# Kernel tuning notes

Hardware: AMD Instinct MI355X
Metric: run time of the kernel (lower is better)

Reference implementation:

```python
import jax, jax.numpy as jnp
import numpy as np
import math

NEIGHBOR_RADIUS = 30.0

def _masked_softmax(logits, mask, axis):
    # mask: bool, True = keep; all-masked rows return zeros
    p = jax.nn.softmax(jnp.where(mask, logits, -1e9), axis=axis) * mask.astype(logits.dtype)
    return p / jnp.clip(jnp.sum(p, axis=axis, keepdims=True), 1e-9, None)

def _forward(agents_state, agents_mask, map_polylines, map_poly_mask,
             map_poly_type, map_tl_status, map_on_route,
             pm_w1, pm_b1, pm_w2, pm_b2, type_emb, tl_emb, route_emb,
             mo_w1, mo_b1, mo_w2, mo_b2,
             ae_w1, ae_b1, ae_w2, ae_b2, ae_w3, ae_b3,
             mr_w1, mr_b1, mr_w2, mr_b2,
             nr_w1, nr_b1, nr_w2, nr_b2,
             to_w1, to_b1, to_w2, to_b2):
    relu = jax.nn.relu
    a_mask = (agents_mask > 0.5).astype(agents_state.dtype)   # (B,N,T)
    a_feat = agents_state[..., :5]
    # ---- map polyline node encoder ----
    h = relu(map_polylines @ pm_w1 + pm_b1)                   # (B,M,L,H)
    h = relu(h @ pm_w2 + pm_b2)
    h = h.max(axis=2)                                         # (B,M,H) max-pool over points
    t_idx = jnp.clip(map_poly_type, 0, type_emb.shape[0] - 1)
    s_idx = jnp.clip(map_tl_status, 0, tl_emb.shape[0] - 1)
    r_idx = jnp.clip(map_on_route, 0, route_emb.shape[0] - 1)
    h = h + type_emb[t_idx] + tl_emb[s_idx] + route_emb[r_idx]
    h = relu(h @ mo_w1 + mo_b1) @ mo_w2 + mo_b2
    map_mask = map_poly_mask > 0.5                            # (B,M) bool
    map_node = h * map_mask[..., None].astype(h.dtype)        # (B,M,D)
    map_center = map_polylines.mean(axis=2)                   # (B,M,2)
    # ---- agent state encoder ----
    a = relu(a_feat @ ae_w1 + ae_b1)
    a = relu(a @ ae_w2 + ae_b2)
    a_emb = (a @ ae_w3 + ae_b3) * a_mask[..., None]           # (B,N,T,D)
    D = a_emb.shape[-1]
    # ---- agent -> map attention ----
    agent_pos = a_feat[..., 0:2]
    rel = map_center[:, None, None, :, :] - agent_pos[:, :, :, None, :]  # (B,N,T,M,2)
    dist = jnp.linalg.norm(rel, axis=-1, keepdims=True)
    rel_feat = jnp.concatenate([rel, dist], axis=-1)          # (B,N,T,M,3)
    rel_score = (relu(rel_feat @ mr_w1 + mr_b1) @ mr_w2 + mr_b2)[..., 0]  # (B,N,T,M)
    dot = jnp.einsum('bntd,bmd->bntm', a_emb, map_node) / math.sqrt(D)
    score_mask = jnp.broadcast_to(map_mask[:, None, None, :], dot.shape)
    attn = _masked_softmax(dot + rel_score, score_mask, axis=-1)
    map_ctx = jnp.einsum('bntm,bmd->bntd', attn, map_node)    # (B,N,T,D)
    # ---- neighbor graph attention ----
    pos = a_feat[..., 0:2]
    vel = a_feat[..., 3:5]
    pos_j = jnp.transpose(pos, (0, 2, 1, 3))                  # (B,T,N,2)
    vel_j = jnp.transpose(vel, (0, 2, 1, 3))
    rel_pos = pos_j[:, None, :, :, :] - pos[:, :, :, None, :] # (B,N,T,N,2) = p_j - p_i
    rel_vel = vel_j[:, None, :, :, :] - vel[:, :, :, None, :]
    dist_ij = jnp.linalg.norm(rel_pos, axis=-1, keepdims=True)
    rel_ij = jnp.concatenate([rel_pos, rel_vel, dist_ij], axis=-1)        # (B,N,T,N,5)
    nbr_score = (relu(rel_ij @ nr_w1 + nr_b1) @ nr_w2 + nr_b2)[..., 0]    # (B,N,T,N)
    am_b = agents_mask > 0.5
    valid_i = am_b[..., None]                                 # (B,N,T,1)
    valid_j = jnp.transpose(am_b, (0, 2, 1))[:, None, :, :]   # (B,1,T,N)
    N = pos.shape[1]
    not_self = ~jnp.eye(N, dtype=bool)[None, :, None, :]      # (1,N,1,N)
    nbr_mask = valid_i & valid_j & (dist_ij[..., 0] <= NEIGHBOR_RADIUS) & not_self
    dot_n = jnp.einsum('bitd,bjtd->bitj', a_emb, a_emb) / math.sqrt(D)
    w_n = _masked_softmax(dot_n + nbr_score, nbr_mask, axis=-1)
    nbr_ctx = jnp.einsum('bitj,bjtd->bitd', w_n, a_emb)       # (B,N,T,D)
    # ---- tau head ----
    tau = jnp.concatenate([a_emb, map_ctx, nbr_ctx], axis=-1)
    tau = relu(tau @ to_w1 + to_b1) @ to_w2 + to_b2
    return tau * a_mask[..., None]

def setup_inputs() -> dict:
    key = jax.random.key(0)
    B, N, T, M, L = 2, 32, 32, 256, 20
    H, D, TAU = 128, 128, 64
    ks = jax.random.split(key, 32)
    def f(i, shp):
        return jax.random.normal(ks[i], shp, jnp.float32) * 0.05
    inp = {}
    inp['agents_state'] = jax.random.normal(ks[0], (B, N, T, 5), jnp.float32) * jnp.array([50., 50., 1., 5., 5.], jnp.float32)
    inp['agents_mask'] = jnp.ones((B, N, T), jnp.float32)
    inp['map_polylines'] = jax.random.normal(ks[1], (B, M, L, 2), jnp.float32) * 50.0
    inp['map_poly_mask'] = jnp.ones((B, M), jnp.float32)
    inp['map_poly_type'] = jax.random.randint(ks[2], (B, M), 0, 4)
    inp['map_tl_status'] = jax.random.randint(ks[3], (B, M), 0, 8)
    inp['map_on_route'] = jax.random.randint(ks[4], (B, M), 0, 2)
    inp['pm_w1'] = f(5, (2, H));  inp['pm_b1'] = jnp.zeros((H,), jnp.float32)
    inp['pm_w2'] = f(6, (H, H)); inp['pm_b2'] = jnp.zeros((H,), jnp.float32)
    inp['type_emb'] = f(7, (4, H)); inp['tl_emb'] = f(8, (8, H)); inp['route_emb'] = f(9, (2, H))
    inp['mo_w1'] = f(10, (H, H)); inp['mo_b1'] = jnp.zeros((H,), jnp.float32)
    inp['mo_w2'] = f(11, (H, D)); inp['mo_b2'] = jnp.zeros((D,), jnp.float32)
    inp['ae_w1'] = f(12, (5, H)); inp['ae_b1'] = jnp.zeros((H,), jnp.float32)
    inp['ae_w2'] = f(13, (H, H)); inp['ae_b2'] = jnp.zeros((H,), jnp.float32)
    inp['ae_w3'] = f(14, (H, D)); inp['ae_b3'] = jnp.zeros((D,), jnp.float32)
    inp['mr_w1'] = f(15, (3, H)); inp['mr_b1'] = jnp.zeros((H,), jnp.float32)
    inp['mr_w2'] = f(16, (H, 1)); inp['mr_b2'] = jnp.zeros((1,), jnp.float32)
    inp['nr_w1'] = f(17, (5, H)); inp['nr_b1'] = jnp.zeros((H,), jnp.float32)
    inp['nr_w2'] = f(18, (H, 1)); inp['nr_b2'] = jnp.zeros((1,), jnp.float32)
    inp['to_w1'] = f(19, (3 * D, H)); inp['to_b1'] = jnp.zeros((H,), jnp.float32)
    inp['to_w2'] = f(20, (H, TAU)); inp['to_b2'] = jnp.zeros((TAU,), jnp.float32)
    return inp

def reference(agents_state, agents_mask, map_polylines, map_poly_mask,
              map_poly_type, map_tl_status, map_on_route,
              pm_w1, pm_b1, pm_w2, pm_b2, type_emb, tl_emb, route_emb,
              mo_w1, mo_b1, mo_w2, mo_b2,
              ae_w1, ae_b1, ae_w2, ae_b2, ae_w3, ae_b3,
              mr_w1, mr_b1, mr_w2, mr_b2,
              nr_w1, nr_b1, nr_w2, nr_b2,
              to_w1, to_b1, to_w2, to_b2):
    return _forward(agents_state, agents_mask, map_polylines, map_poly_mask,
                    map_poly_type, map_tl_status, map_on_route,
                    pm_w1, pm_b1, pm_w2, pm_b2, type_emb, tl_emb, route_emb,
                    mo_w1, mo_b1, mo_w2, mo_b2,
                    ae_w1, ae_b1, ae_w2, ae_b2, ae_w3, ae_b3,
                    mr_w1, mr_b1, mr_w2, mr_b2,
                    nr_w1, nr_b1, nr_w2, nr_b2,
                    to_w1, to_b1, to_w2, to_b2)
```

## Files before the change

### kernel.cpp

```cpp
#include <hip/hip_runtime.h>

#define RSQRT_D 0.08838834764831843f

__global__ __launch_bounds__(256) void kAB_front(
    const float* __restrict__ poly, const float* __restrict__ pmask,
    const int* __restrict__ ptype, const int* __restrict__ ptl, const int* __restrict__ proute,
    const float* __restrict__ pm_w1, const float* __restrict__ pm_b1,
    const float* __restrict__ pm_w2, const float* __restrict__ pm_b2,
    const float* __restrict__ type_emb, const float* __restrict__ tl_emb, const float* __restrict__ route_emb,
    const float* __restrict__ mo_w1, const float* __restrict__ mo_b1,
    const float* __restrict__ mo_w2, const float* __restrict__ mo_b2,
    const float* __restrict__ astate, const float* __restrict__ amask,
    const float* __restrict__ ae_w1, const float* __restrict__ ae_b1,
    const float* __restrict__ ae_w2, const float* __restrict__ ae_b2,
    const float* __restrict__ ae_w3, const float* __restrict__ ae_b3,
    float* __restrict__ map_node, float* __restrict__ map_nodeT, float* __restrict__ center,
    float* __restrict__ a_emb, float* __restrict__ aT, float* __restrict__ posT)
{
    int tid = threadIdx.x;
    if (blockIdx.x < 512) {
        int bm = blockIdx.x;
        int b = bm >> 8, m = bm & 255;
        int h = tid & 127, rw = tid >> 7;
        __shared__ float xch[2][128];
        __shared__ __align__(16) float hvs[128];
        __shared__ __align__(16) float g2[128];

        const float* pp = poly + bm*40 + rw*20;
        float xs[10], ys[10];
        #pragma unroll
        for (int u = 0; u < 10; ++u) { xs[u] = pp[2*u]; ys[u] = pp[2*u+1]; }
        float acc[10];
        #pragma unroll
        for (int u = 0; u < 10; ++u) acc[u] = 0.f;
        #pragma unroll 4
        for (int k = 0; k < 128; ++k) {
            float w2v = pm_w2[k*128 + h];
            float wx = pm_w1[k], wy = pm_w1[128+k], bb = pm_b1[k];
            #pragma unroll
            for (int u = 0; u < 10; ++u) {
                float h1 = fmaxf(fmaf(wx, xs[u], fmaf(wy, ys[u], bb)), 0.f);
                acc[u] = fmaf(h1, w2v, acc[u]);
            }
        }
        float mx = acc[0];
        #pragma unroll
        for (int u = 1; u < 10; ++u) mx = fmaxf(mx, acc[u]);
        xch[rw][h] = mx;
        __syncthreads();
        if (rw == 0) {
            float v = fmaxf(fmaxf(mx, xch[1][h]) + pm_b2[h], 0.f);
            int ti = min(max(ptype[bm],0),3);
            int si = min(max(ptl[bm],0),7);
            int ri = min(max(proute[bm],0),1);
            hvs[h] = v + type_emb[ti*128+h] + tl_emb[si*128+h] + route_emb[ri*128+h];
        }
        __syncthreads();
        if (rw == 0) {
            float a1 = mo_b1[h];
            for (int kc = 0; kc < 32; ++kc) {
                float4 xv = *(const float4*)&hvs[kc*4];
                a1 = fmaf(xv.x, mo_w1[(kc*4+0)*128+h],
                     fmaf(xv.y, mo_w1[(kc*4+1)*128+h],
                     fmaf(xv.z, mo_w1[(kc*4+2)*128+h],
                     fmaf(xv.w, mo_w1[(kc*4+3)*128+h], a1))));
            }
            g2[h] = fmaxf(a1, 0.f);
        }
        __syncthreads();
        if (rw == 0) {
            float a2 = mo_b2[h];
            for (int kc = 0; kc < 32; ++kc) {
                float4 xv = *(const float4*)&g2[kc*4];
                a2 = fmaf(xv.x, mo_w2[(kc*4+0)*128+h],
                     fmaf(xv.y, mo_w2[(kc*4+1)*128+h],
                     fmaf(xv.z, mo_w2[(kc*4+2)*128+h],
                     fmaf(xv.w, mo_w2[(kc*4+3)*128+h], a2))));
            }
            float mk = (pmask[bm] > 0.5f) ? 1.f : 0.f;
            a2 *= mk;
            map_node[bm*128 + h] = a2;
            map_nodeT[(b*128+h)*256 + m] = a2;
        }
        if (tid == 0) {
            float sx = 0.f, sy = 0.f;
            #pragma unroll
            for (int l = 0; l < 20; ++l) { sx += poly[bm*40 + 2*l]; sy += poly[bm*40 + 2*l + 1]; }
            center[bm*2+0] = sx * 0.05f;
            center[bm*2+1] = sy * 0.05f;
        }
    } else {
        int h = tid & 127, rp = tid >> 7;
        int r0 = (blockIdx.x - 512)*8 + rp*4;
        __shared__ float f5[2][4][5];
        __shared__ __align__(16) float a1s[2][4][128];
        if (h < 20) f5[rp][h/5][h%5] = astate[(r0 + h/5)*5 + (h%5)];
        __syncthreads();
        float b1v = ae_b1[h];
        float v[4];
        {
            float w0 = ae_w1[h], w1 = ae_w1[128+h], w2 = ae_w1[256+h], w3 = ae_w1[384+h], w4 = ae_w1[512+h];
            #pragma unroll
            for (int r = 0; r < 4; ++r) {
                float a = b1v;
                a = fmaf(f5[rp][r][0], w0, a); a = fmaf(f5[rp][r][1], w1, a);
                a = fmaf(f5[rp][r][2], w2, a); a = fmaf(f5[rp][r][3], w3, a);
                a = fmaf(f5[rp][r][4], w4, a);
                v[r] = fmaxf(a, 0.f);
            }
        }
        #pragma unroll
        for (int r = 0; r < 4; ++r) a1s[rp][r][h] = v[r];
        __syncthreads();
        {
            float b2v = ae_b2[h];
            float a0 = b2v, a1 = b2v, a2 = b2v, a3 = b2v;
            for (int kc = 0; kc < 32; ++kc) {
                float4 x0 = *(const float4*)&a1s[rp][0][kc*4];
                float4 x1 = *(const float4*)&a1s[rp][1][kc*4];
                float4 x2 = *(const float4*)&a1s[rp][2][kc*4];
                float4 x3 = *(const float4*)&a1s[rp][3][kc*4];
                float w0 = ae_w2[(kc*4+0)*128+h], w1 = ae_w2[(kc*4+1)*128+h];
                float w2 = ae_w2[(kc*4+2)*128+h], w3 = ae_w2[(kc*4+3)*128+h];
                a0 = fmaf(x0.x,w0,fmaf(x0.y,w1,fmaf(x0.z,w2,fmaf(x0.w,w3,a0))));
                a1 = fmaf(x1.x,w0,fmaf(x1.y,w1,fmaf(x1.z,w2,fmaf(x1.w,w3,a1))));
                a2 = fmaf(x2.x,w0,fmaf(x2.y,w1,fmaf(x2.z,w2,fmaf(x2.w,w3,a2))));
                a3 = fmaf(x3.x,w0,fmaf(x3.y,w1,fmaf(x3.z,w2,fmaf(x3.w,w3,a3))));
            }
            v[0]=fmaxf(a0,0.f); v[1]=fmaxf(a1,0.f); v[2]=fmaxf(a2,0.f); v[3]=fmaxf(a3,0.f);
        }
        __syncthreads();
        #pragma unroll
        for (int r = 0; r < 4; ++r) a1s[rp][r][h] = v[r];
        __syncthreads();
        {
            float b3v = ae_b3[h];
            float a0 = b3v, a1 = b3v, a2 = b3v, a3 = b3v;
            for (int kc = 0; kc < 32; ++kc) {
                float4 x0 = *(const float4*)&a1s[rp][0][kc*4];
                float4 x1 = *(const float4*)&a1s[rp][1][kc*4];
                float4 x2 = *(const float4*)&a1s[rp][2][kc*4];
                float4 x3 = *(const float4*)&a1s[rp][3][kc*4];
                float w0 = ae_w3[(kc*4+0)*128+h], w1 = ae_w3[(kc*4+1)*128+h];
                float w2 = ae_w3[(kc*4+2)*128+h], w3 = ae_w3[(kc*4+3)*128+h];
                a0 = fmaf(x0.x,w0,fmaf(x0.y,w1,fmaf(x0.z,w2,fmaf(x0.w,w3,a0))));
                a1 = fmaf(x1.x,w0,fmaf(x1.y,w1,fmaf(x1.z,w2,fmaf(x1.w,w3,a1))));
                a2 = fmaf(x2.x,w0,fmaf(x2.y,w1,fmaf(x2.z,w2,fmaf(x2.w,w3,a2))));
                a3 = fmaf(x3.x,w0,fmaf(x3.y,w1,fmaf(x3.z,w2,fmaf(x3.w,w3,a3))));
            }
            v[0]=a0; v[1]=a1; v[2]=a2; v[3]=a3;
        }
        #pragma unroll
        for (int r = 0; r < 4; ++r) {
            int rr = r0 + r;
            float mk = (amask[rr] > 0.5f) ? 1.f : 0.f;
            float e = v[r] * mk;
            a_emb[rr*128 + h] = e;
            int bb = rr >> 10, nn = (rr >> 5) & 31, tt = rr & 31;
            int bt = bb*32 + tt;
            aT[(bt*128 + h)*32 + nn] = e;
        }
        if (h < 20) {
            int r = h / 5, c = h % 5;
            int rr = r0 + r;
            int bb = rr >> 10, nn = (rr >> 5) & 31, tt = rr & 31;
            int bt = bb*32 + tt;
            float val;
            if      (c == 0) val = f5[rp][r][0];
            else if (c == 1) val = f5[rp][r][1];
            else if (c == 2) val = f5[rp][r][3];
            else if (c == 3) val = f5[rp][r][4];
            else             val = amask[rr];
            posT[(bt*5 + c)*32 + nn] = val;
        }
    }
}

__global__ __launch_bounds__(256) void kC_attn(
    const float* __restrict__ astate, const float* __restrict__ amask,
    const float* __restrict__ pmask,
    const float* __restrict__ a_emb, const float* __restrict__ map_node,
    const float* __restrict__ map_nodeT, const float* __restrict__ center,
    const float* __restrict__ mr_w1, const float* __restrict__ mr_b1,
    const float* __restrict__ mr_w2, const float* __restrict__ mr_b2,
    const float* __restrict__ aT, const float* __restrict__ posT,
    const float* __restrict__ nr_w1, const float* __restrict__ nr_b1,
    const float* __restrict__ nr_w2, const float* __restrict__ nr_b2,
    float* __restrict__ map_ctx, float* __restrict__ p_n)
{
    int tid = threadIdx.x;
    int lam = tid & 63, wv = tid >> 6;
    __shared__ float lg4[4][256];
    __shared__ __align__(16) float p4[256*4];
    __shared__ float ctxp[4][128];

    if (blockIdx.x < 512) {
        int r0 = blockIdx.x * 4;
        int b = r0 >> 10;
        int m = tid;
        float rx[4], ry[4], dd[4], dt[4], sA[4];
        float b2c = mr_b2[0];
        float cx = center[(b*256+m)*2+0], cy = center[(b*256+m)*2+1];
        #pragma unroll
        for (int r = 0; r < 4; ++r) {
            float px = astate[(r0+r)*5+0], py = astate[(r0+r)*5+1];
            rx[r] = cx - px; ry[r] = cy - py;
            dd[r] = sqrtf(rx[r]*rx[r] + ry[r]*ry[r]);
            dt[r] = 0.f; sA[r] = b2c;
        }
        #pragma unroll 8
        for (int hh = 0; hh < 128; ++hh) {
            float wa = mr_w1[hh], wb = mr_w1[128+hh], wc = mr_w1[256+hh];
            float bb = mr_b1[hh], w2 = mr_w2[hh];
            #pragma unroll
            for (int r = 0; r < 4; ++r) {
                float t1 = fmaf(rx[r], wa, fmaf(ry[r], wb, fmaf(dd[r], wc, bb)));
                sA[r] = fmaf(fmaxf(t1, 0.f), w2, sA[r]);
            }
        }
        const float* mT = map_nodeT + b*128*256 + m;
        #pragma unroll 8
        for (int d = 0; d < 128; ++d) {
            float v = mT[d*256];
            #pragma unroll
            for (int r = 0; r < 4; ++r)
                dt[r] = fmaf(v, a_emb[(r0+r)*128 + d], dt[r]);
        }
        bool mk = pmask[b*256+m] > 0.5f;
        #pragma unroll
        for (int r = 0; r < 4; ++r)
            lg4[r][m] = mk ? fmaf(dt[r], RSQRT_D, sA[r]) : -1e30f;
        __syncthreads();
        {
            float x0 = lg4[wv][lam], x1 = lg4[wv][64+lam], x2 = lg4[wv][128+lam], x3 = lg4[wv][192+lam];
            float mxv = fmaxf(fmaxf(x0,x1), fmaxf(x2,x3));
            #pragma unroll
            for (int off = 32; off; off >>= 1) mxv = fmaxf(mxv, __shfl_xor(mxv, off));
            float e0 = (x0 > -1e29f) ? expf(x0-mxv) : 0.f;
            float e1 = (x1 > -1e29f) ? expf(x1-mxv) : 0.f;
            float e2 = (x2 > -1e29f) ? expf(x2-mxv) : 0.f;
            float e3 = (x3 > -1e29f) ? expf(x3-mxv) : 0.f;
            float sm = e0+e1+e2+e3;
            #pragma unroll
            for (int off = 32; off; off >>= 1) sm += __shfl_xor(sm, off);
            float inv = 1.f / fmaxf(sm, 1e-9f);
            p4[lam*4 + wv]       = e0*inv;
            p4[(64+lam)*4 + wv]  = e1*inv;
            p4[(128+lam)*4 + wv] = e2*inv;
            p4[(192+lam)*4 + wv] = e3*inv;
        }
        __syncthreads();
        {
            int d = tid & 127, hf = tid >> 7;
            float ac0 = 0.f, ac1 = 0.f, ac2 = 0.f, ac3 = 0.f;
            const float* mn = map_node + (b*256 + hf*128)*128 + d;
            const float4* pp = (const float4*)p4 + hf*128;
            #pragma unroll 4
            for (int mm = 0; mm < 128; ++mm) {
                float4 pv = pp[mm];
                float v = mn[mm*128];
                ac0 = fmaf(pv.x, v, ac0); ac1 = fmaf(pv.y, v, ac1);
                ac2 = fmaf(pv.z, v, ac2); ac3 = fmaf(pv.w, v, ac3);
            }
            if (hf == 1) { ctxp[0][d]=ac0; ctxp[1][d]=ac1; ctxp[2][d]=ac2; ctxp[3][d]=ac3; }
            __syncthreads();
            if (hf == 0) {
                map_ctx[(r0+0)*128+d] = ac0 + ctxp[0][d];
                map_ctx[(r0+1)*128+d] = ac1 + ctxp[1][d];
                map_ctx[(r0+2)*128+d] = ac2 + ctxp[2][d];
                map_ctx[(r0+3)*128+d] = ac3 + ctxp[3][d];
            }
        }
    } else {
        int r = (blockIdx.x - 512)*4 + wv;
        int b = r >> 10, ii = (r >> 5) & 31, tt = r & 31;
        int bt = b*32 + tt;
        int j = lam & 31, hs = lam >> 5;
        float pxi = astate[r*5+0], pyi = astate[r*5+1], vxi = astate[r*5+3], vyi = astate[r*5+4];
        const float* pT = posT + bt*160;
        float pxj = pT[j], pyj = pT[32+j], vxj = pT[64+j], vyj = pT[96+j], mj = pT[128+j];
        float rpx = pxj-pxi, rpy = pyj-pyi, rvx = vxj-vxi, rvy = vyj-vyi;
        float ddv = sqrtf(rpx*rpx + rpy*rpy);
        const float* ei = a_emb + (size_t)r*128;
        const float* aTp = aT + (size_t)bt*4096 + j;
        float s = 0.f, dot = 0.f;
        int h0 = hs*64;
        #pragma unroll 8
        for (int q = 0; q < 64; ++q) {
            int hh = h0 + q;
            float wA = nr_w1[hh], wB = nr_w1[128+hh], wC = nr_w1[256+hh];
            float wD = nr_w1[384+hh], wE = nr_w1[512+hh];
            float bb = nr_b1[hh], w2 = nr_w2[hh];
            float t1 = fmaf(rpx, wA, fmaf(rpy, wB, fmaf(rvx, wC,
                       fmaf(rvy, wD, fmaf(ddv, wE, bb)))));
            s = fmaf(fmaxf(t1, 0.f), w2, s);
            dot = fmaf(ei[hh], aTp[hh*32], dot);
        }
        s   += __shfl_xor(s, 32);
        dot += __shfl_xor(dot, 32);
        bool vi = amask[r] > 0.5f, vj = mj > 0.5f;
        bool ok = vi && vj && (ddv <= 30.0f) && (j != ii);
        float lg = ok ? fmaf(dot, RSQRT_D, s + nr_b2[0]) : -1e30f;
        float mxv = lg;
        #pragma unroll
        for (int off = 16; off; off >>= 1) mxv = fmaxf(mxv, __shfl_xor(mxv, off));
        float e = (lg > -1e29f) ? expf(lg - mxv) : 0.f;
        float sm = e;
        #pragma unroll
        for (int off = 16; off; off >>= 1) sm += __shfl_xor(sm, off);
        if (hs == 0) p_n[r*32 + j] = e / fmaxf(sm, 1e-9f);
    }
}

__global__ __launch_bounds__(256) void kD_out(
    const float* __restrict__ amask, const float* __restrict__ a_emb,
    const float* __restrict__ map_ctx, const float* __restrict__ p_n,
    const float* __restrict__ to_w1, const float* __restrict__ to_b1,
    const float* __restrict__ to_w2, const float* __restrict__ to_b2,
    float* __restrict__ out)
{
    int r0 = blockIdx.x * 4;
    int b = r0 >> 10, t0 = r0 & 31;
    int tid = threadIdx.x;
    __shared__ __align__(16) float tau[4][384];
    __shared__ float redn[4][128];
    __shared__ __align__(16) float gpart[4][4][128];
    __shared__ __align__(16) float g1s[4][128];

    for (int q = tid; q < 512; q += 256) {
        int rr = q >> 7, d = q & 127;
        tau[rr][d]       = a_emb[(r0+rr)*128 + d];
        tau[rr][128 + d] = map_ctx[(r0+rr)*128 + d];
    }
    __syncthreads();
    {
        int d = tid & 127, hf = tid >> 7;
        float ac[4] = {0.f,0.f,0.f,0.f};
        for (int jj = 0; jj < 16; ++jj) {
            int j2 = hf*16 + jj;
            float p0 = p_n[(r0+0)*32 + j2];
            float p1 = p_n[(r0+1)*32 + j2];
            float p2 = p_n[(r0+2)*32 + j2];
            float p3 = p_n[(r0+3)*32 + j2];
            const float* ejb = a_emb + (size_t)((b*32 + j2)*32 + t0)*128 + d;
            ac[0] = fmaf(p0, ejb[0],   ac[0]);
            ac[1] = fmaf(p1, ejb[128], ac[1]);
            ac[2] = fmaf(p2, ejb[256], ac[2]);
            ac[3] = fmaf(p3, ejb[384], ac[3]);
        }
        if (hf == 1) { redn[0][d]=ac[0]; redn[1][d]=ac[1]; redn[2][d]=ac[2]; redn[3][d]=ac[3]; }
        __syncthreads();
        if (hf == 0) {
            #pragma unroll
            for (int r = 0; r < 4; ++r) tau[r][256 + d] = ac[r] + redn[r][d];
        }
    }
    __syncthreads();
    {
        int h6 = tid & 63, kq = tid >> 6;
        float aL[4] = {0.f,0.f,0.f,0.f};
        float aH[4] = {0.f,0.f,0.f,0.f};
        for (int c = 0; c < 24; ++c) {
            int k4 = kq*24 + c;
            float4 x0 = *(const float4*)&tau[0][k4*4];
            float4 x1 = *(const float4*)&tau[1][k4*4];
            float4 x2 = *(const float4*)&tau[2][k4*4];
            float4 x3 = *(const float4*)&tau[3][k4*4];
            float wl0 = to_w1[(k4*4+0)*128 + h6], wh0 = to_w1[(k4*4+0)*128 + 64+h6];
            float wl1 = to_w1[(k4*4+1)*128 + h6], wh1 = to_w1[(k4*4+1)*128 + 64+h6];
            float wl2 = to_w1[(k4*4+2)*128 + h6], wh2 = to_w1[(k4*4+2)*128 + 64+h6];
            float wl3 = to_w1[(k4*4+3)*128 + h6], wh3 = to_w1[(k4*4+3)*128 + 64+h6];
            aL[0]=fmaf(x0.x,wl0,fmaf(x0.y,wl1,fmaf(x0.z,wl2,fmaf(x0.w,wl3,aL[0]))));
            aH[0]=fmaf(x0.x,wh0,fmaf(x0.y,wh1,fmaf(x0.z,wh2,fmaf(x0.w,wh3,aH[0]))));
            aL[1]=fmaf(x1.x,wl0,fmaf(x1.y,wl1,fmaf(x1.z,wl2,fmaf(x1.w,wl3,aL[1]))));
            aH[1]=fmaf(x1.x,wh0,fmaf(x1.y,wh1,fmaf(x1.z,wh2,fmaf(x1.w,wh3,aH[1]))));
            aL[2]=fmaf(x2.x,wl0,fmaf(x2.y,wl1,fmaf(x2.z,wl2,fmaf(x2.w,wl3,aL[2]))));
            aH[2]=fmaf(x2.x,wh0,fmaf(x2.y,wh1,fmaf(x2.z,wh2,fmaf(x2.w,wh3,aH[2]))));
            aL[3]=fmaf(x3.x,wl0,fmaf(x3.y,wl1,fmaf(x3.z,wl2,fmaf(x3.w,wl3,aL[3]))));
            aH[3]=fmaf(x3.x,wh0,fmaf(x3.y,wh1,fmaf(x3.z,wh2,fmaf(x3.w,wh3,aH[3]))));
        }
        #pragma unroll
        for (int r = 0; r < 4; ++r) {
            gpart[kq][r][h6]      = aL[r];
            gpart[kq][r][64 + h6] = aH[r];
        }
    }
    __syncthreads();
    {
        int h = tid & 127, rp = tid >> 7;
        float bv = to_b1[h];
        #pragma unroll
        for (int rr = rp; rr < 4; rr += 2) {
            float s = gpart[0][rr][h] + gpart[1][rr][h] + gpart[2][rr][h] + gpart[3][rr][h];
            g1s[rr][h] = fmaxf(s + bv, 0.f);
        }
    }
    __syncthreads();
    {
        int o = tid & 63, row = tid >> 6;
        float a2 = to_b2[o];
        for (int kc = 0; kc < 32; ++kc) {
            float4 g = *(const float4*)&g1s[row][kc*4];
            a2 = fmaf(g.x, to_w2[(kc*4+0)*64 + o],
                 fmaf(g.y, to_w2[(kc*4+1)*64 + o],
                 fmaf(g.z, to_w2[(kc*4+2)*64 + o],
                 fmaf(g.w, to_w2[(kc*4+3)*64 + o], a2))));
        }
        float mk = (amask[r0+row] > 0.5f) ? 1.f : 0.f;
        out[(r0+row)*64 + o] = a2 * mk;
    }
}

extern "C" void kernel_launch(void* const* d_in, const int* in_sizes, int n_in,
                              void* d_out, int out_size, void* d_ws, size_t ws_size,
                              hipStream_t stream) {
    const float* agents_state  = (const float*)d_in[0];
    const float* agents_mask   = (const float*)d_in[1];
    const float* map_polylines = (const float*)d_in[2];
    const float* map_poly_mask = (const float*)d_in[3];
    const int*   map_poly_type = (const int*)d_in[4];
    const int*   map_tl_status = (const int*)d_in[5];
    const int*   map_on_route  = (const int*)d_in[6];
    const float* pm_w1 = (const float*)d_in[7];
    const float* pm_b1 = (const float*)d_in[8];
    const float* pm_w2 = (const float*)d_in[9];
    const float* pm_b2 = (const float*)d_in[10];
    const float* type_emb  = (const float*)d_in[11];
    const float* tl_emb    = (const float*)d_in[12];
    const float* route_emb = (const float*)d_in[13];
    const float* mo_w1 = (const float*)d_in[14];
    const float* mo_b1 = (const float*)d_in[15];
    const float* mo_w2 = (const float*)d_in[16];
    const float* mo_b2 = (const float*)d_in[17];
    const float* ae_w1 = (const float*)d_in[18];
    const float* ae_b1 = (const float*)d_in[19];
    const float* ae_w2 = (const float*)d_in[20];
    const float* ae_b2 = (const float*)d_in[21];
    const float* ae_w3 = (const float*)d_in[22];
    const float* ae_b3 = (const float*)d_in[23];
    const float* mr_w1 = (const float*)d_in[24];
    const float* mr_b1 = (const float*)d_in[25];
    const float* mr_w2 = (const float*)d_in[26];
    const float* mr_b2 = (const float*)d_in[27];
    const float* nr_w1 = (const float*)d_in[28];
    const float* nr_b1 = (const float*)d_in[29];
    const float* nr_w2 = (const float*)d_in[30];
    const float* nr_b2 = (const float*)d_in[31];
    const float* to_w1 = (const float*)d_in[32];
    const float* to_b1 = (const float*)d_in[33];
    const float* to_w2 = (const float*)d_in[34];
    const float* to_b2 = (const float*)d_in[35];

    float* ws = (float*)d_ws;
    float* map_node  = ws;
    float* map_nodeT = ws + 65536;
    float* center    = ws + 131072;
    float* a_emb     = ws + 132096;
    float* aT        = ws + 394240;
    float* posT      = ws + 656384;
    float* map_ctx   = ws + 666624;
    float* p_n       = ws + 928768;

    float* out = (float*)d_out;

    kAB_front<<<768, 256, 0, stream>>>(map_polylines, map_poly_mask,
        map_poly_type, map_tl_status, map_on_route,
        pm_w1, pm_b1, pm_w2, pm_b2, type_emb, tl_emb, route_emb,
        mo_w1, mo_b1, mo_w2, mo_b2,
        agents_state, agents_mask,
        ae_w1, ae_b1, ae_w2, ae_b2, ae_w3, ae_b3,
        map_node, map_nodeT, center, a_emb, aT, posT);

    kC_attn<<<1024, 256, 0, stream>>>(agents_state, agents_mask, map_poly_mask,
        a_emb, map_node, map_nodeT, center,
        mr_w1, mr_b1, mr_w2, mr_b2,
        aT, posT,
        nr_w1, nr_b1, nr_w2, nr_b2,
        map_ctx, p_n);

    kD_out<<<512, 256, 0, stream>>>(agents_mask, a_emb, map_ctx, p_n,
        to_w1, to_b1, to_w2, to_b2, out);
}
```

Before: 189.6 us.

## Fuse agent attention and output head into one per-row-block kernel

Merges the map-attention, neighbor-attention and output MLP kernels into a single kernel with 512 blocks, each handling four agent rows end to end. Map context and neighbor probabilities stay in shared memory instead of being written to and re-read from global workspace, and one kernel launch is removed. The cost is fewer blocks, each running longer and using more shared memory, which may lower occupancy and remove the parallelism previously gained from splitting the map and neighbor work across separate blocks.

```diff
diff --git a/kernel.cpp b/kernel.cpp
--- a/kernel.cpp
+++ b/kernel.cpp
@@ -176,7 +176,7 @@
     }
 }
 
-__global__ __launch_bounds__(256) void kC_attn(
+__global__ __launch_bounds__(256) void kBack(
     const float* __restrict__ astate, const float* __restrict__ amask,
     const float* __restrict__ pmask,
     const float* __restrict__ a_emb, const float* __restrict__ map_node,
@@ -186,94 +186,27 @@
     const float* __restrict__ aT, const float* __restrict__ posT,
     const float* __restrict__ nr_w1, const float* __restrict__ nr_b1,
     const float* __restrict__ nr_w2, const float* __restrict__ nr_b2,
-    float* __restrict__ map_ctx, float* __restrict__ p_n)
+    const float* __restrict__ to_w1, const float* __restrict__ to_b1,
+    const float* __restrict__ to_w2, const float* __restrict__ to_b2,
+    float* __restrict__ out)
 {
     int tid = threadIdx.x;
     int lam = tid & 63, wv = tid >> 6;
+    int r0 = blockIdx.x * 4;
+    int b = r0 >> 10, t0 = r0 & 31;
+
     __shared__ float lg4[4][256];
     __shared__ __align__(16) float p4[256*4];
     __shared__ float ctxp[4][128];
-
-    if (blockIdx.x < 512) {
-        int r0 = blockIdx.x * 4;
-        int b = r0 >> 10;
-        int m = tid;
-        float rx[4], ry[4], dd[4], dt[4], sA[4];
-        float b2c = mr_b2[0];
-        float cx = center[(b*256+m)*2+0], cy = center[(b*256+m)*2+1];
-        #pragma unroll
-        for (int r = 0; r < 4; ++r) {
-            float px = astate[(r0+r)*5+0], py = astate[(r0+r)*5+1];
-            rx[r] = cx - px; ry[r] = cy - py;
-            dd[r] = sqrtf(rx[r]*rx[r] + ry[r]*ry[r]);
-            dt[r] = 0.f; sA[r] = b2c;
-        }
-        #pragma unroll 8
-        for (int hh = 0; hh < 128; ++hh) {
-            float wa = mr_w1[hh], wb = mr_w1[128+hh], wc = mr_w1[256+hh];
-            float bb = mr_b1[hh], w2 = mr_w2[hh];
-            #pragma unroll
-            for (int r = 0; r < 4; ++r) {
-                float t1 = fmaf(rx[r], wa, fmaf(ry[r], wb, fmaf(dd[r], wc, bb)));
-                sA[r] = fmaf(fmaxf(t1, 0.f), w2, sA[r]);
-            }
-        }
-        const float* mT = map_nodeT + b*128*256 + m;
-        #pragma unroll 8
-        for (int d = 0; d < 128; ++d) {
-            float v = mT[d*256];
-            #pragma unroll
-            for (int r = 0; r < 4; ++r)
-                dt[r] = fmaf(v, a_emb[(r0+r)*128 + d], dt[r]);
-        }
-        bool mk = pmask[b*256+m] > 0.5f;
-        #pragma unroll
-        for (int r = 0; r < 4; ++r)
-            lg4[r][m] = mk ? fmaf(dt[r], RSQRT_D, sA[r]) : -1e30f;
-        __syncthreads();
-        {
-            float x0 = lg4[wv][lam], x1 = lg4[wv][64+lam], x2 = lg4[wv][128+lam], x3 = lg4[wv][192+lam];
-            float mxv = fmaxf(fmaxf(x0,x1), fmaxf(x2,x3));
-            #pragma unroll
-            for (int off = 32; off; off >>= 1) mxv = fmaxf(mxv, __shfl_xor(mxv, off));
-            float e0 = (x0 > -1e29f) ? expf(x0-mxv) : 0.f;
-            float e1 = (x1 > -1e29f) ? expf(x1-mxv) : 0.f;
-            float e2 = (x2 > -1e29f) ? expf(x2-mxv) : 0.f;
-            float e3 = (x3 > -1e29f) ? expf(x3-mxv) : 0.f;
-            float sm = e0+e1+e2+e3;
-            #pragma unroll
-            for (int off = 32; off; off >>= 1) sm += __shfl_xor(sm, off);
-            float inv = 1.f / fmaxf(sm, 1e-9f);
-            p4[lam*4 + wv]       = e0*inv;
-            p4[(64+lam)*4 + wv]  = e1*inv;
-            p4[(128+lam)*4 + wv] = e2*inv;
-            p4[(192+lam)*4 + wv] = e3*inv;
-        }
-        __syncthreads();
-        {
-            int d = tid & 127, hf = tid >> 7;
-            float ac0 = 0.f, ac1 = 0.f, ac2 = 0.f, ac3 = 0.f;
-            const float* mn = map_node + (b*256 + hf*128)*128 + d;
-            const float4* pp = (const float4*)p4 + hf*128;
-            #pragma unroll 4
-            for (int mm = 0; mm < 128; ++mm) {
-                float4 pv = pp[mm];
-                float v = mn[mm*128];
-                ac0 = fmaf(pv.x, v, ac0); ac1 = fmaf(pv.y, v, ac1);
-                ac2 = fmaf(pv.z, v, ac2); ac3 = fmaf(pv.w, v, ac3);
-            }
-            if (hf == 1) { ctxp[0][d]=ac0; ctxp[1][d]=ac1; ctxp[2][d]=ac2; ctxp[3][d]=ac3; }
-            __syncthreads();
-            if (hf == 0) {
-                map_ctx[(r0+0)*128+d] = ac0 + ctxp[0][d];
-                map_ctx[(r0+1)*128+d] = ac1 + ctxp[1][d];
-                map_ctx[(r0+2)*128+d] = ac2 + ctxp[2][d];
-                map_ctx[(r0+3)*128+d] = ac3 + ctxp[3][d];
-            }
-        }
-    } else {
-        int r = (blockIdx.x - 512)*4 + wv;
-        int b = r >> 10, ii = (r >> 5) & 31, tt = r & 31;
+    __shared__ float p_loc[4][32];
+    __shared__ __align__(16) float tau[4][384];
+    __shared__ float redn[4][128];
+    __shared__ __align__(16) float gpart[4][4][128];
+    __shared__ __align__(16) float g1s[4][128];
+
+    {
+        int r = r0 + wv;
+        int ii = (r >> 5) & 31, tt = r & 31;
         int bt = b*32 + tt;
         int j = lam & 31, hs = lam >> 5;
         float pxi = astate[r*5+0], pyi = astate[r*5+1], vxi = astate[r*5+3], vyi = astate[r*5+4];
@@ -308,40 +241,101 @@
         float sm = e;
         #pragma unroll
         for (int off = 16; off; off >>= 1) sm += __shfl_xor(sm, off);
-        if (hs == 0) p_n[r*32 + j] = e / fmaxf(sm, 1e-9f);
-    }
-}
-
-__global__ __launch_bounds__(256) void kD_out(
-    const float* __restrict__ amask, const float* __restrict__ a_emb,
-    const float* __restrict__ map_ctx, const float* __restrict__ p_n,
-    const float* __restrict__ to_w1, const float* __restrict__ to_b1,
-    const float* __restrict__ to_w2, const float* __restrict__ to_b2,
-    float* __restrict__ out)
-{
-    int r0 = blockIdx.x * 4;
-    int b = r0 >> 10, t0 = r0 & 31;
-    int tid = threadIdx.x;
-    __shared__ __align__(16) float tau[4][384];
-    __shared__ float redn[4][128];
-    __shared__ __align__(16) float gpart[4][4][128];
-    __shared__ __align__(16) float g1s[4][128];
-
-    for (int q = tid; q < 512; q += 256) {
-        int rr = q >> 7, d = q & 127;
-        tau[rr][d]       = a_emb[(r0+rr)*128 + d];
-        tau[rr][128 + d] = map_ctx[(r0+rr)*128 + d];
-    }
-    __syncthreads();
+        if (hs == 0) p_loc[wv][j] = e / fmaxf(sm, 1e-9f);
+    }
+
+    {
+        int m = tid;
+        float rx[4], ry[4], dd[4], dt[4], sA[4];
+        float b2c = mr_b2[0];
+        float cx = center[(b*256+m)*2+0], cy = center[(b*256+m)*2+1];
+        #pragma unroll
+        for (int r = 0; r < 4; ++r) {
+            float px = astate[(r0+r)*5+0], py = astate[(r0+r)*5+1];
+            rx[r] = cx - px; ry[r] = cy - py;
+            dd[r] = sqrtf(rx[r]*rx[r] + ry[r]*ry[r]);
+            dt[r] = 0.f; sA[r] = b2c;
+        }
+        #pragma unroll 8
+        for (int hh = 0; hh < 128; ++hh) {
+            float wa = mr_w1[hh], wb = mr_w1[128+hh], wc = mr_w1[256+hh];
+            float bb = mr_b1[hh], w2 = mr_w2[hh];
+            #pragma unroll
+            for (int r = 0; r < 4; ++r) {
+                float t1 = fmaf(rx[r], wa, fmaf(ry[r], wb, fmaf(dd[r], wc, bb)));
+                sA[r] = fmaf(fmaxf(t1, 0.f), w2, sA[r]);
+            }
+        }
+        const float* mT = map_nodeT + b*128*256 + m;
+        #pragma unroll 8
+        for (int d = 0; d < 128; ++d) {
+            float v = mT[d*256];
+            #pragma unroll
+            for (int r = 0; r < 4; ++r)
+                dt[r] = fmaf(v, a_emb[(r0+r)*128 + d], dt[r]);
+        }
+        bool mk = pmask[b*256+m] > 0.5f;
+        #pragma unroll
+        for (int r = 0; r < 4; ++r)
+            lg4[r][m] = mk ? fmaf(dt[r], RSQRT_D, sA[r]) : -1e30f;
+    }
+    __syncthreads();
+
+    {
+        float x0 = lg4[wv][lam], x1 = lg4[wv][64+lam], x2 = lg4[wv][128+lam], x3 = lg4[wv][192+lam];
+        float mxv = fmaxf(fmaxf(x0,x1), fmaxf(x2,x3));
+        #pragma unroll
+        for (int off = 32; off; off >>= 1) mxv = fmaxf(mxv, __shfl_xor(mxv, off));
+        float e0 = (x0 > -1e29f) ? expf(x0-mxv) : 0.f;
+        float e1 = (x1 > -1e29f) ? expf(x1-mxv) : 0.f;
+        float e2 = (x2 > -1e29f) ? expf(x2-mxv) : 0.f;
+        float e3 = (x3 > -1e29f) ? expf(x3-mxv) : 0.f;
+        float sm = e0+e1+e2+e3;
+        #pragma unroll
+        for (int off = 32; off; off >>= 1) sm += __shfl_xor(sm, off);
+        float inv = 1.f / fmaxf(sm, 1e-9f);
+        p4[lam*4 + wv]       = e0*inv;
+        p4[(64+lam)*4 + wv]  = e1*inv;
+        p4[(128+lam)*4 + wv] = e2*inv;
+        p4[(192+lam)*4 + wv] = e3*inv;
+    }
+    __syncthreads();
+
+    {
+        int d = tid & 127, hf = tid >> 7;
+        float ac0 = 0.f, ac1 = 0.f, ac2 = 0.f, ac3 = 0.f;
+        const float* mn = map_node + (b*256 + hf*128)*128 + d;
+        const float4* pp = (const float4*)p4 + hf*128;
+        #pragma unroll 4
+        for (int mm = 0; mm < 128; ++mm) {
+            float4 pv = pp[mm];
+            float v = mn[mm*128];
+            ac0 = fmaf(pv.x, v, ac0); ac1 = fmaf(pv.y, v, ac1);
+            ac2 = fmaf(pv.z, v, ac2); ac3 = fmaf(pv.w, v, ac3);
+        }
+        if (hf == 1) { ctxp[0][d]=ac0; ctxp[1][d]=ac1; ctxp[2][d]=ac2; ctxp[3][d]=ac3; }
+        #pragma unroll
+        for (int r = hf; r < 4; r += 2)
+            tau[r][d] = a_emb[(r0+r)*128 + d];
+        __syncthreads();
+        if (hf == 0) {
+            tau[0][128+d] = ac0 + ctxp[0][d];
+            tau[1][128+d] = ac1 + ctxp[1][d];
+            tau[2][128+d] = ac2 + ctxp[2][d];
+            tau[3][128+d] = ac3 + ctxp[3][d];
+        }
+    }
+    __syncthreads();
+
     {
         int d = tid & 127, hf = tid >> 7;
         float ac[4] = {0.f,0.f,0.f,0.f};
         for (int jj = 0; jj < 16; ++jj) {
             int j2 = hf*16 + jj;
-            float p0 = p_n[(r0+0)*32 + j2];
-            float p1 = p_n[(r0+1)*32 + j2];
-            float p2 = p_n[(r0+2)*32 + j2];
-            float p3 = p_n[(r0+3)*32 + j2];
+            float p0 = p_loc[0][j2];
+            float p1 = p_loc[1][j2];
+            float p2 = p_loc[2][j2];
+            float p3 = p_loc[3][j2];
             const float* ejb = a_emb + (size_t)((b*32 + j2)*32 + t0)*128 + d;
             ac[0] = fmaf(p0, ejb[0],   ac[0]);
             ac[1] = fmaf(p1, ejb[128], ac[1]);
@@ -356,6 +350,7 @@
         }
     }
     __syncthreads();
+
     {
         int h6 = tid & 63, kq = tid >> 6;
         float aL[4] = {0.f,0.f,0.f,0.f};
@@ -458,8 +453,6 @@
     float* a_emb     = ws + 132096;
     float* aT        = ws + 394240;
     float* posT      = ws + 656384;
-    float* map_ctx   = ws + 666624;
-    float* p_n       = ws + 928768;
 
     float* out = (float*)d_out;
 
@@ -471,13 +464,10 @@
         ae_w1, ae_b1, ae_w2, ae_b2, ae_w3, ae_b3,
         map_node, map_nodeT, center, a_emb, aT, posT);
 
-    kC_attn<<<1024, 256, 0, stream>>>(agents_state, agents_mask, map_poly_mask,
+    kBack<<<512, 256, 0, stream>>>(agents_state, agents_mask, map_poly_mask,
         a_emb, map_node, map_nodeT, center,
         mr_w1, mr_b1, mr_w2, mr_b2,
         aT, posT,
         nr_w1, nr_b1, nr_w2, nr_b2,
-        map_ctx, p_n);
-
-    kD_out<<<512, 256, 0, stream>>>(agents_mask, a_emb, map_ctx, p_n,
         to_w1, to_b1, to_w2, to_b2, out);
 }
```

Result: no change. 191.4 us (+1.0%).

## Double kC_attn block size and split hidden/feature reductions across thread halves

Applied to the files above, without the earlier changes.

kC_attn now runs 512-thread blocks. In the map-attention branch, the two thread halves each compute half of the relation-MLP hidden units and half of the dot-product dimensions, and the partial logits are combined through shared memory. The context accumulation is split four ways over map nodes. The neighbor branch handles 8 agent rows per block, so the grid shrinks from 1024 to 768 blocks. The goal is more parallelism per row group and shorter serial loops, at the cost of extra syncs, shared-memory partial buffers, and idle threads during the softmax.

```diff
diff --git a/kernel.cpp b/kernel.cpp
--- a/kernel.cpp
+++ b/kernel.cpp
@@ -176,7 +176,7 @@
     }
 }
 
-__global__ __launch_bounds__(256) void kC_attn(
+__global__ __launch_bounds__(512) void kC_attn(
     const float* __restrict__ astate, const float* __restrict__ amask,
     const float* __restrict__ pmask,
     const float* __restrict__ a_emb, const float* __restrict__ map_node,
@@ -190,48 +190,60 @@
 {
     int tid = threadIdx.x;
     int lam = tid & 63, wv = tid >> 6;
+    __shared__ float lgp[2][4][256];
     __shared__ float lg4[4][256];
     __shared__ __align__(16) float p4[256*4];
-    __shared__ float ctxp[4][128];
+    __shared__ float ctxp[4][4][128];
 
     if (blockIdx.x < 512) {
         int r0 = blockIdx.x * 4;
         int b = r0 >> 10;
-        int m = tid;
-        float rx[4], ry[4], dd[4], dt[4], sA[4];
-        float b2c = mr_b2[0];
-        float cx = center[(b*256+m)*2+0], cy = center[(b*256+m)*2+1];
-        #pragma unroll
-        for (int r = 0; r < 4; ++r) {
-            float px = astate[(r0+r)*5+0], py = astate[(r0+r)*5+1];
-            rx[r] = cx - px; ry[r] = cy - py;
-            dd[r] = sqrtf(rx[r]*rx[r] + ry[r]*ry[r]);
-            dt[r] = 0.f; sA[r] = b2c;
-        }
-        #pragma unroll 8
-        for (int hh = 0; hh < 128; ++hh) {
-            float wa = mr_w1[hh], wb = mr_w1[128+hh], wc = mr_w1[256+hh];
-            float bb = mr_b1[hh], w2 = mr_w2[hh];
+        int m = tid & 255, hf = tid >> 8;
+        int h0 = hf * 64;
+        {
+            float rx[4], ry[4], dd[4], dt[4], sA[4];
+            float b2c = (hf == 0) ? mr_b2[0] : 0.f;
+            float cx = center[(b*256+m)*2+0], cy = center[(b*256+m)*2+1];
             #pragma unroll
             for (int r = 0; r < 4; ++r) {
-                float t1 = fmaf(rx[r], wa, fmaf(ry[r], wb, fmaf(dd[r], wc, bb)));
-                sA[r] = fmaf(fmaxf(t1, 0.f), w2, sA[r]);
-            }
-        }
-        const float* mT = map_nodeT + b*128*256 + m;
-        #pragma unroll 8
-        for (int d = 0; d < 128; ++d) {
-            float v = mT[d*256];
+                float px = astate[(r0+r)*5+0], py = astate[(r0+r)*5+1];
+                rx[r] = cx - px; ry[r] = cy - py;
+                dd[r] = sqrtf(rx[r]*rx[r] + ry[r]*ry[r]);
+                dt[r] = 0.f; sA[r] = b2c;
+            }
+            #pragma unroll 8
+            for (int q = 0; q < 64; ++q) {
+                int hh = h0 + q;
+                float wa = mr_w1[hh], wb = mr_w1[128+hh], wc = mr_w1[256+hh];
+                float bb = mr_b1[hh], w2 = mr_w2[hh];
+                #pragma unroll
+                for (int r = 0; r < 4; ++r) {
+                    float t1 = fmaf(rx[r], wa, fmaf(ry[r], wb, fmaf(dd[r], wc, bb)));
+                    sA[r] = fmaf(fmaxf(t1, 0.f), w2, sA[r]);
+                }
+            }
+            const float* mT = map_nodeT + b*128*256 + m;
+            #pragma unroll 8
+            for (int q = 0; q < 64; ++q) {
+                int d = h0 + q;
+                float v = mT[d*256];
+                #pragma unroll
+                for (int r = 0; r < 4; ++r)
+                    dt[r] = fmaf(v, a_emb[(r0+r)*128 + d], dt[r]);
+            }
             #pragma unroll
             for (int r = 0; r < 4; ++r)
-                dt[r] = fmaf(v, a_emb[(r0+r)*128 + d], dt[r]);
-        }
-        bool mk = pmask[b*256+m] > 0.5f;
-        #pragma unroll
-        for (int r = 0; r < 4; ++r)
-            lg4[r][m] = mk ? fmaf(dt[r], RSQRT_D, sA[r]) : -1e30f;
-        __syncthreads();
-        {
+                lgp[hf][r][m] = fmaf(dt[r], RSQRT_D, sA[r]);
+        }
+        __syncthreads();
+        if (hf == 0) {
+            bool mk = pmask[b*256+m] > 0.5f;
+            #pragma unroll
+            for (int r = 0; r < 4; ++r)
+                lg4[r][m] = mk ? (lgp[0][r][m] + lgp[1][r][m]) : -1e30f;
+        }
+        __syncthreads();
+        if (tid < 256) {
             float x0 = lg4[wv][lam], x1 = lg4[wv][64+lam], x2 = lg4[wv][128+lam], x3 = lg4[wv][192+lam];
             float mxv = fmaxf(fmaxf(x0,x1), fmaxf(x2,x3));
             #pragma unroll
@@ -251,28 +263,28 @@
         }
         __syncthreads();
         {
-            int d = tid & 127, hf = tid >> 7;
+            int d = tid & 127, q = tid >> 7;
             float ac0 = 0.f, ac1 = 0.f, ac2 = 0.f, ac3 = 0.f;
-            const float* mn = map_node + (b*256 + hf*128)*128 + d;
-            const float4* pp = (const float4*)p4 + hf*128;
+            const float* mn = map_node + (b*256 + q*64)*128 + d;
+            const float4* pp = (const float4*)p4 + q*64;
             #pragma unroll 4
-            for (int mm = 0; mm < 128; ++mm) {
+            for (int mm = 0; mm < 64; ++mm) {
                 float4 pv = pp[mm];
                 float v = mn[mm*128];
                 ac0 = fmaf(pv.x, v, ac0); ac1 = fmaf(pv.y, v, ac1);
                 ac2 = fmaf(pv.z, v, ac2); ac3 = fmaf(pv.w, v, ac3);
             }
-            if (hf == 1) { ctxp[0][d]=ac0; ctxp[1][d]=ac1; ctxp[2][d]=ac2; ctxp[3][d]=ac3; }
-            __syncthreads();
-            if (hf == 0) {
-                map_ctx[(r0+0)*128+d] = ac0 + ctxp[0][d];
-                map_ctx[(r0+1)*128+d] = ac1 + ctxp[1][d];
-                map_ctx[(r0+2)*128+d] = ac2 + ctxp[2][d];
-                map_ctx[(r0+3)*128+d] = ac3 + ctxp[3][d];
-            }
+            ctxp[q][0][d] = ac0; ctxp[q][1][d] = ac1;
+            ctxp[q][2][d] = ac2; ctxp[q][3][d] = ac3;
+        }
+        __syncthreads();
+        {
+            int d = tid & 127, r = tid >> 7;
+            map_ctx[(r0+r)*128 + d] =
+                ctxp[0][r][d] + ctxp[1][r][d] + ctxp[2][r][d] + ctxp[3][r][d];
         }
     } else {
-        int r = (blockIdx.x - 512)*4 + wv;
+        int r = (blockIdx.x - 512)*8 + wv;
         int b = r >> 10, ii = (r >> 5) & 31, tt = r & 31;
         int bt = b*32 + tt;
         int j = lam & 31, hs = lam >> 5;
@@ -471,7 +483,7 @@
         ae_w1, ae_b1, ae_w2, ae_b2, ae_w3, ae_b3,
         map_node, map_nodeT, center, a_emb, aT, posT);
 
-    kC_attn<<<1024, 256, 0, stream>>>(agents_state, agents_mask, map_poly_mask,
+    kC_attn<<<768, 512, 0, stream>>>(agents_state, agents_mask, map_poly_mask,
         a_emb, map_node, map_nodeT, center,
         mr_w1, mr_b1, mr_w2, mr_b2,
         aT, posT,
```

New measurement: 196.2 us. 3.5% more time.
